# Kernel tuning notes

Measured on AMD Instinct MI355X. Metric: run time of the kernel, lower is better.

Reference implementation:

```python
import jax, jax.numpy as jnp
import numpy as np

B, S, H = 2, 2048, 2048
NH, NKV, HD = 16, 4, 128  # heads, kv heads, head_dim
GROUP = NH // NKV
THETA = 10000.0
NEG = -1e9


def _rope_tables(seq_len, head_dim, theta):
    inv_freq = 1.0 / (theta ** (jnp.arange(0, head_dim, 2, dtype=jnp.float32) / head_dim))
    t = jnp.arange(seq_len, dtype=jnp.float32)
    freqs = jnp.outer(t, inv_freq)                 # [S, HD/2]
    emb = jnp.concatenate([freqs, freqs], axis=-1)  # [S, HD]
    return jnp.cos(emb), jnp.sin(emb)


def _rotate_half(x):
    half = x.shape[-1] // 2
    return jnp.concatenate([-x[..., half:], x[..., :half]], axis=-1)


def setup_inputs() -> dict:
    key = jax.random.key(0)
    ks = jax.random.split(key, 5)
    scale = 0.02
    x = jax.random.normal(ks[0], (B, S, H), dtype=jnp.float32)
    Wq = jax.random.normal(ks[1], (NH * HD, H), dtype=jnp.float32) * scale
    Wk = jax.random.normal(ks[2], (NKV * HD, H), dtype=jnp.float32) * scale
    Wv = jax.random.normal(ks[3], (NKV * HD, H), dtype=jnp.float32) * scale
    Wo = jax.random.normal(ks[4], (H, NH * HD), dtype=jnp.float32) * scale
    cos, sin = _rope_tables(S, HD, THETA)
    # additive causal mask: 0 on/below diagonal, -1e9 above
    causal = jnp.triu(jnp.full((S, S), NEG, dtype=jnp.float32), k=1)
    mask = causal[None, None]  # [1,1,S,S]
    return {"x": x, "Wq": Wq, "Wk": Wk, "Wv": Wv, "Wo": Wo,
            "cos": cos, "sin": sin, "mask": mask}


def reference(x, Wq, Wk, Wv, Wo, cos, sin, mask):
    b, s, _ = x.shape
    # projections (nn.Linear, no bias): y = x @ W.T
    q = (x @ Wq.T).reshape(b, s, NH, HD).transpose(0, 2, 1, 3)    # [B,NH,S,D]
    k = (x @ Wk.T).reshape(b, s, NKV, HD).transpose(0, 2, 1, 3)   # [B,NKV,S,D]
    v = (x @ Wv.T).reshape(b, s, NKV, HD).transpose(0, 2, 1, 3)   # [B,NKV,S,D]
    # RoPE
    c = cos[None, None]  # [1,1,S,D]
    sn = sin[None, None]
    q = q * c + _rotate_half(q) * sn
    k = k * c + _rotate_half(k) * sn
    # GQA: repeat KV heads to match query heads (mirrors _repeat_kv)
    k = jnp.repeat(k, GROUP, axis=1)  # [B,NH,S,D]
    v = jnp.repeat(v, GROUP, axis=1)
    # scaled dot-product attention with additive mask
    scores = jnp.einsum('bhqd,bhkd->bhqk', q, k) / jnp.sqrt(jnp.float32(HD))
    scores = scores + mask
    p = jax.nn.softmax(scores, axis=-1)
    ctx = jnp.einsum('bhqk,bhkd->bhqd', p, v)            # [B,NH,S,D]
    ctx = ctx.transpose(0, 2, 1, 3).reshape(b, s, NH * HD)
    return ctx @ Wo.T
```

## Files before the change

### kernel.cpp

```cpp
#include <hip/hip_runtime.h>
#include <stdint.h>

#define B_   2
#define S_   2048
#define H_   2048
#define NH_  16
#define NKV_ 4
#define HD_  128
#define M_   (B_ * S_)

typedef short bf16x8 __attribute__((ext_vector_type(8)));
typedef float f32x4  __attribute__((ext_vector_type(4)));
typedef float f32x16 __attribute__((ext_vector_type(16)));

__device__ __forceinline__ float b2f(unsigned short u) {
  union { unsigned int u; float f; } v; v.u = ((unsigned int)u) << 16; return v.f;
}
__device__ __forceinline__ unsigned short f2b(float f) {
  union { float f; unsigned int u; } v; v.f = f;
  unsigned int u = v.u;
  unsigned int r = (u + 0x7FFFu + ((u >> 16) & 1u)) >> 16;
  return (unsigned short)r;
}
__device__ __forceinline__ uint4 pack8(const float4& a, const float4& b) {
  uint4 r;
  r.x = (unsigned)f2b(a.x) | ((unsigned)f2b(a.y) << 16);
  r.y = (unsigned)f2b(a.z) | ((unsigned)f2b(a.w) << 16);
  r.z = (unsigned)f2b(b.x) | ((unsigned)f2b(b.y) << 16);
  r.w = (unsigned)f2b(b.z) | ((unsigned)f2b(b.w) << 16);
  return r;
}
__device__ __forceinline__ void gload_lds(const unsigned short* g, unsigned short* l) {
  __builtin_amdgcn_global_load_lds(
      (const __attribute__((address_space(1))) unsigned int*)g,
      (__attribute__((address_space(3))) unsigned int*)l, 16, 0, 0);
}

__global__ void cvt_bf16(const float* __restrict__ src, unsigned short* __restrict__ dst, int n8)
{
  int i = blockIdx.x * blockDim.x + threadIdx.x;
  if (i >= n8) return;
  const float* p = src + (size_t)i * 8;
  uint4 v = pack8(*reinterpret_cast<const float4*>(p), *reinterpret_cast<const float4*>(p + 4));
  *reinterpret_cast<uint4*>(dst + (size_t)i * 8) = v;
}

template<bool CF32>
__global__ __launch_bounds__(256, 4) void gemm_ld(
    const unsigned short* __restrict__ A, const unsigned short* __restrict__ B0,
    const unsigned short* __restrict__ B1, void* __restrict__ C0, void* __restrict__ C1,
    int N, int K, int nxHalf)
{
  __shared__ unsigned short As[128 * 64];
  __shared__ unsigned short Bs[128 * 64];

  const unsigned short* Bm; void* Cm; int colBase;
  if ((int)blockIdx.x < nxHalf) { Bm = B0; Cm = C0; colBase = blockIdx.x * 128; }
  else                          { Bm = B1; Cm = C1; colBase = (blockIdx.x - nxHalf) * 128; }
  const int rowBase = blockIdx.y * 128;

  const int tid    = threadIdx.x;
  const int lane   = tid & 63;
  const int wid    = tid >> 6;
  const int wrow   = wid >> 1;
  const int wcol   = wid & 1;
  const int lane15 = lane & 15;
  const int quad   = lane >> 4;

  const f32x4 zero = {0.f, 0.f, 0.f, 0.f};
  f32x4 acc[4][4];
#pragma unroll
  for (int i = 0; i < 4; i++)
#pragma unroll
    for (int j = 0; j < 4; j++) acc[i][j] = zero;

  const int lr  = lane >> 3;
  const int sc8 = (lane & 7) ^ lr;

  for (int kb = 0; kb < K; kb += 64) {
    __syncthreads();
#pragma unroll
    for (int i = 0; i < 4; i++) {
      const int rg = (i * 4 + wid) * 8;
      const int r  = rg + lr;
      gload_lds(A  + (size_t)(rowBase + r) * K + kb + sc8 * 8, As + rg * 64);
      gload_lds(Bm + (size_t)(colBase + r) * K + kb + sc8 * 8, Bs + rg * 64);
    }
    __syncthreads();
#pragma unroll
    for (int kc = 0; kc < 2; kc++) {
      bf16x8 af[4], bf[4];
#pragma unroll
      for (int g = 0; g < 4; g++) {
        const int ra = wrow * 64 + g * 16 + lane15;
        const int rb = wcol * 64 + g * 16 + lane15;
        af[g] = *reinterpret_cast<const bf16x8*>(As + ra * 64 + (((kc * 4 + quad) ^ (ra & 7)) * 8));
        bf[g] = *reinterpret_cast<const bf16x8*>(Bs + rb * 64 + (((kc * 4 + quad) ^ (rb & 7)) * 8));
      }
#pragma unroll
      for (int i = 0; i < 4; i++)
#pragma unroll
        for (int j = 0; j < 4; j++)
          acc[i][j] = __builtin_amdgcn_mfma_f32_16x16x32_bf16(af[i], bf[j], acc[i][j], 0, 0, 0);
    }
  }

  if (CF32) {
    float* Cf = (float*)Cm;
#pragma unroll
    for (int i = 0; i < 4; i++) {
      int row = rowBase + wrow * 64 + i * 16 + quad * 4;
#pragma unroll
      for (int j = 0; j < 4; j++) {
        int col = colBase + wcol * 64 + j * 16 + lane15;
#pragma unroll
        for (int rr = 0; rr < 4; rr++)
          Cf[(size_t)(row + rr) * N + col] = acc[i][j][rr];
      }
    }
  } else {
    unsigned short* Cb = (unsigned short*)Cm;
#pragma unroll
    for (int i = 0; i < 4; i++) {
      int row = rowBase + wrow * 64 + i * 16 + quad * 4;
#pragma unroll
      for (int j = 0; j < 4; j++) {
        int col = colBase + wcol * 64 + j * 16 + lane15;
#pragma unroll
        for (int rr = 0; rr < 4; rr++)
          Cb[(size_t)(row + rr) * N + col] = f2b(acc[i][j][rr]);
      }
    }
  }
}

template<bool OPROJ>
__global__ __launch_bounds__(256, 3) void gemm_k(
    const void* __restrict__ A, const float* __restrict__ B0, const float* __restrict__ B1,
    void* __restrict__ C0, void* __restrict__ C1, int N, int K, int nxHalf)
{
  __shared__ unsigned short As[128 * 72];
  __shared__ unsigned short Bs[128 * 72];

  const float* Bm; void* Cm; int colBase;
  if ((int)blockIdx.x < nxHalf) { Bm = B0; Cm = C0; colBase = blockIdx.x * 128; }
  else                          { Bm = B1; Cm = C1; colBase = (blockIdx.x - nxHalf) * 128; }
  const int rowBase = blockIdx.y * 128;

  const int tid    = threadIdx.x;
  const int lane   = tid & 63;
  const int wid    = tid >> 6;
  const int wrow   = wid >> 1;
  const int wcol   = wid & 1;
  const int lane15 = lane & 15;
  const int quad   = lane >> 4;

  const f32x4 zero = {0.f, 0.f, 0.f, 0.f};
  f32x4 acc[4][4];
#pragma unroll
  for (int i = 0; i < 4; i++)
#pragma unroll
    for (int j = 0; j < 4; j++) acc[i][j] = zero;

  const int r0 = tid >> 3;
  const int c8 = tid & 7;

  uint4 av[4], bv[4];
#pragma unroll
  for (int p = 0; p < 4; p++) {
    int r = r0 + 32 * p;
    if (OPROJ) {
      av[p] = *reinterpret_cast<const uint4*>((const unsigned short*)A + (size_t)(rowBase + r) * K + c8 * 8);
    } else {
      const float* pA = (const float*)A + (size_t)(rowBase + r) * K + c8 * 8;
      av[p] = pack8(*reinterpret_cast<const float4*>(pA), *reinterpret_cast<const float4*>(pA + 4));
    }
    const float* pB = Bm + (size_t)(colBase + r) * K + c8 * 8;
    bv[p] = pack8(*reinterpret_cast<const float4*>(pB), *reinterpret_cast<const float4*>(pB + 4));
  }

  for (int kb = 0; kb < K; kb += 64) {
    __syncthreads();
#pragma unroll
    for (int p = 0; p < 4; p++) {
      int r = r0 + 32 * p;
      *reinterpret_cast<uint4*>(As + r * 72 + c8 * 8) = av[p];
      *reinterpret_cast<uint4*>(Bs + r * 72 + c8 * 8) = bv[p];
    }
    __syncthreads();
    const int kn = kb + 64;
    if (kn < K) {
#pragma unroll
      for (int p = 0; p < 4; p++) {
        int r = r0 + 32 * p;
        if (OPROJ) {
          av[p] = *reinterpret_cast<const uint4*>((const unsigned short*)A + (size_t)(rowBase + r) * K + kn + c8 * 8);
        } else {
          const float* pA = (const float*)A + (size_t)(rowBase + r) * K + kn + c8 * 8;
          av[p] = pack8(*reinterpret_cast<const float4*>(pA), *reinterpret_cast<const float4*>(pA + 4));
        }
        const float* pB = Bm + (size_t)(colBase + r) * K + kn + c8 * 8;
        bv[p] = pack8(*reinterpret_cast<const float4*>(pB), *reinterpret_cast<const float4*>(pB + 4));
      }
    }
#pragma unroll
    for (int kc = 0; kc < 2; kc++) {
      bf16x8 af[4], bf[4];
#pragma unroll
      for (int g = 0; g < 4; g++) {
        af[g] = *reinterpret_cast<const bf16x8*>(As + (wrow * 64 + g * 16 + lane15) * 72 + kc * 32 + quad * 8);
        bf[g] = *reinterpret_cast<const bf16x8*>(Bs + (wcol * 64 + g * 16 + lane15) * 72 + kc * 32 + quad * 8);
      }
#pragma unroll
      for (int i = 0; i < 4; i++)
#pragma unroll
        for (int j = 0; j < 4; j++)
          acc[i][j] = __builtin_amdgcn_mfma_f32_16x16x32_bf16(af[i], bf[j], acc[i][j], 0, 0, 0);
    }
  }

  if (OPROJ) {
    float* Cf = (float*)Cm;
#pragma unroll
    for (int i = 0; i < 4; i++) {
      int row = rowBase + wrow * 64 + i * 16 + quad * 4;
#pragma unroll
      for (int j = 0; j < 4; j++) {
        int col = colBase + wcol * 64 + j * 16 + lane15;
#pragma unroll
        for (int rr = 0; rr < 4; rr++)
          Cf[(size_t)(row + rr) * N + col] = acc[i][j][rr];
      }
    }
  } else {
    unsigned short* Cb = (unsigned short*)Cm;
#pragma unroll
    for (int i = 0; i < 4; i++) {
      int row = rowBase + wrow * 64 + i * 16 + quad * 4;
#pragma unroll
      for (int j = 0; j < 4; j++) {
        int col = colBase + wcol * 64 + j * 16 + lane15;
#pragma unroll
        for (int rr = 0; rr < 4; rr++)
          Cb[(size_t)(row + rr) * N + col] = f2b(acc[i][j][rr]);
      }
    }
  }
}

__global__ void rope_k(unsigned short* __restrict__ Qb, unsigned short* __restrict__ Kb,
                       const float* __restrict__ cosT, const float* __restrict__ sinT)
{
  const int per_tok = (NH_ + NKV_) * 64;
  int idx = blockIdx.x * blockDim.x + threadIdx.x;
  int t = idx / per_tok;
  int r = idx - t * per_tok;
  if (t >= M_) return;
  int s = t & (S_ - 1);
  unsigned short* base;
  int d;
  if (r < NH_ * 64) {
    int h = r >> 6; d = r & 63;
    base = Qb + (size_t)t * (NH_ * HD_) + h * HD_ + d;
  } else {
    int rk = r - NH_ * 64;
    int h = rk >> 6; d = rk & 63;
    base = Kb + (size_t)t * (NKV_ * HD_) + h * HD_ + d;
  }
  float c  = cosT[s * HD_ + d];
  float sn = sinT[s * HD_ + d];
  float x0 = b2f(base[0]);
  float x1 = b2f(base[64]);
  base[0]  = f2b(x0 * c - x1 * sn);
  base[64] = f2b(x1 * c + x0 * sn);
}

__global__ void transp_v(const unsigned short* __restrict__ Vb, unsigned short* __restrict__ VT)
{
  __shared__ unsigned short Ls[64 * 72];
  const int t0 = blockIdx.x * 64;
  const int d0 = blockIdx.y * 64;
  const int tid = threadIdx.x;
  const int r = tid >> 3, c = tid & 7;
#pragma unroll
  for (int p = 0; p < 2; p++)
    *reinterpret_cast<uint4*>(Ls + (r + 32 * p) * 72 + c * 8) =
      *reinterpret_cast<const uint4*>(Vb + (size_t)(t0 + r + 32 * p) * (NKV_ * HD_) + d0 + c * 8);
  __syncthreads();
  const int bq = t0 >> 11, s0 = t0 & (S_ - 1);
#pragma unroll
  for (int p = 0; p < 2; p++) {
    int dl = r + 32 * p;
    unsigned short tmp[8];
#pragma unroll
    for (int j = 0; j < 8; j++) tmp[j] = Ls[(c * 8 + j) * 72 + dl];
    *reinterpret_cast<uint4*>(VT + (size_t)(bq * 512 + d0 + dl) * S_ + s0 + c * 8) =
      *reinterpret_cast<uint4*>(tmp);
  }
}

__global__ __launch_bounds__(512, 2) void attn(
    const unsigned short* __restrict__ Q, const unsigned short* __restrict__ Kc,
    const unsigned short* __restrict__ VT, unsigned short* __restrict__ O)
{
  __shared__ unsigned short Ks[64 * 128];
  __shared__ unsigned short Vs[128 * 64];
  __shared__ float Ll[8 * 32];

  const int tid  = threadIdx.x;
  const int lane = tid & 63;
  const int w    = tid >> 6;
  const int l31  = lane & 31;
  const int hi   = lane >> 5;
  const int qt   = blockIdx.x;
  const int kvh  = blockIdx.y;
  const int b    = blockIdx.z;
  const int h    = kvh * 4 + (w & 3);
  const int rg   = w >> 2;
  const size_t bS = (size_t)b * S_;
  const int ntot = qt + 1;

  const int kr   = tid >> 4;
  const int kc16 = tid & 15;
  const int vd   = tid >> 3;
  const int vc8  = tid & 7;

  const unsigned short* Kbase = Kc + bS * (NKV_ * HD_) + kvh * HD_;
  const unsigned short* Vbase = VT + (size_t)(b * 512 + kvh * HD_) * S_;

  bf16x8 qf[8];
  {
    const unsigned short* qp = Q + (bS + qt * 64 + rg * 32 + l31) * (NH_ * HD_) + h * HD_ + hi * 8;
#pragma unroll
    for (int kc = 0; kc < 8; kc++) qf[kc] = *reinterpret_cast<const bf16x8*>(qp + kc * 16);
  }

  f32x16 ctx[4];
#pragma unroll
  for (int ng = 0; ng < 4; ng++)
#pragma unroll
    for (int r = 0; r < 16; r++) ctx[ng][r] = 0.f;
  float lsum = 0.f;

  uint4 kreg[2], vreg[2];
#pragma unroll
  for (int p2 = 0; p2 < 2; p2++) {
    kreg[p2] = *reinterpret_cast<const uint4*>(Kbase + (size_t)(kr + 32 * p2) * (NKV_ * HD_) + kc16 * 8);
    vreg[p2] = *reinterpret_cast<const uint4*>(Vbase + (size_t)(vd + 64 * p2) * S_ + vc8 * 8);
  }

  const float scale = 0.08838834764831845f;

  for (int kt = 0; kt < ntot; kt++) {
    __syncthreads();
#pragma unroll
    for (int p2 = 0; p2 < 2; p2++) {
      const int row = kr + 32 * p2;
      *reinterpret_cast<uint4*>(Ks + row * 128 + ((kc16 ^ (row & 15)) * 8)) = kreg[p2];
      const int d = vd + 64 * p2;
      *reinterpret_cast<uint4*>(Vs + d * 64 + ((vc8 ^ (d & 7)) * 8)) = vreg[p2];
    }
    __syncthreads();

    if (kt + 1 < ntot) {
      const int key0 = (kt + 1) * 64;
#pragma unroll
      for (int p2 = 0; p2 < 2; p2++) {
        kreg[p2] = *reinterpret_cast<const uint4*>(Kbase + (size_t)(key0 + kr + 32 * p2) * (NKV_ * HD_) + kc16 * 8);
        vreg[p2] = *reinterpret_cast<const uint4*>(Vbase + (size_t)(vd + 64 * p2) * S_ + key0 + vc8 * 8);
      }
    }

    f32x16 sc0, sc1;
#pragma unroll
    for (int r = 0; r < 16; r++) { sc0[r] = 0.f; sc1[r] = 0.f; }
#pragma unroll
    for (int kc = 0; kc < 8; kc++) {
      const int ch = ((kc * 2 + hi) ^ (l31 & 15)) * 8;
      bf16x8 kf0 = *reinterpret_cast<const bf16x8*>(Ks + l31 * 128 + ch);
      sc0 = __builtin_amdgcn_mfma_f32_32x32x16_bf16(kf0, qf[kc], sc0, 0, 0, 0);
      bf16x8 kf1 = *reinterpret_cast<const bf16x8*>(Ks + (32 + l31) * 128 + ch);
      sc1 = __builtin_amdgcn_mfma_f32_32x32x16_bf16(kf1, qf[kc], sc1, 0, 0, 0);
    }

    const int lim = (kt == qt) ? (rg * 32 + l31) : 4096;
    bf16x8 pfrag[4];
#pragma unroll
    for (int cg = 0; cg < 2; cg++) {
      float pe[16];
#pragma unroll
      for (int r = 0; r < 16; r++) {
        float v = (cg ? sc1[r] : sc0[r]) * scale;
        const int kp = cg * 32 + (r & 3) + 8 * (r >> 2) + 4 * hi;
        v = (kp <= lim) ? v : -1.0e9f;
        float e = __expf(v);
        pe[r] = e;
        lsum += e;
      }
      unsigned wd[8];
#pragma unroll
      for (int j = 0; j < 8; j++) {
        unsigned t;
        asm("v_cvt_pk_bf16_f32 %0, %1, %2" : "=v"(t) : "v"(pe[2 * j]), "v"(pe[2 * j + 1]));
        wd[j] = t;
      }
      asm("v_permlane32_swap_b32 %0, %1" : "+v"(wd[0]), "+v"(wd[2]));
      asm("v_permlane32_swap_b32 %0, %1" : "+v"(wd[1]), "+v"(wd[3]));
      asm("v_permlane32_swap_b32 %0, %1" : "+v"(wd[4]), "+v"(wd[6]));
      asm("v_permlane32_swap_b32 %0, %1" : "+v"(wd[5]), "+v"(wd[7]));
      union { unsigned u[4]; bf16x8 v8; } ua, ub;
      ua.u[0] = wd[0]; ua.u[1] = wd[1]; ua.u[2] = wd[2]; ua.u[3] = wd[3];
      ub.u[0] = wd[4]; ub.u[1] = wd[5]; ub.u[2] = wd[6]; ub.u[3] = wd[7];
      pfrag[cg * 2]     = ua.v8;
      pfrag[cg * 2 + 1] = ub.v8;
    }

#pragma unroll
    for (int ng = 0; ng < 4; ng++) {
      const int drow = ng * 32 + l31;
#pragma unroll
      for (int kc = 0; kc < 4; kc++) {
        bf16x8 vf = *reinterpret_cast<const bf16x8*>(Vs + drow * 64 + (((kc * 2 + hi) ^ (l31 & 7)) * 8));
        ctx[ng] = __builtin_amdgcn_mfma_f32_32x32x16_bf16(pfrag[kc], vf, ctx[ng], 0, 0, 0);
      }
    }
  }

  {
    float lt = lsum + __shfl_xor(lsum, 32);
    Ll[w * 32 + l31] = 1.0f / lt;
  }
  f32x4 iv[4];
#pragma unroll
  for (int g = 0; g < 4; g++)
    iv[g] = *reinterpret_cast<const f32x4*>(&Ll[w * 32 + 4 * hi + 8 * g]);

  const size_t orow0 = bS + qt * 64 + rg * 32;
#pragma unroll
  for (int ng = 0; ng < 4; ng++) {
#pragma unroll
    for (int r = 0; r < 16; r++) {
      const int qp = (r & 3) + 8 * (r >> 2) + 4 * hi;
      O[(orow0 + qp) * (NH_ * HD_) + h * HD_ + ng * 32 + l31] = f2b(ctx[ng][r] * iv[r >> 2][r & 3]);
    }
  }
}

extern "C" void kernel_launch(void* const* d_in, const int* in_sizes, int n_in,
                              void* d_out, int out_size, void* d_ws, size_t ws_size,
                              hipStream_t stream) {
  const float* x    = (const float*)d_in[0];
  const float* Wq   = (const float*)d_in[1];
  const float* Wk   = (const float*)d_in[2];
  const float* Wv   = (const float*)d_in[3];
  const float* Wo   = (const float*)d_in[4];
  const float* cosT = (const float*)d_in[5];
  const float* sinT = (const float*)d_in[6];
  float* out = (float*)d_out;

  const size_t qElems  = (size_t)M_ * NH_ * HD_;
  const size_t xElems  = (size_t)M_ * H_;
  const size_t wqElems = (size_t)H_ * H_;
  const size_t wkElems = (size_t)NKV_ * HD_ * H_;
  const size_t bigNeed = (qElems + xElems + 2 * wqElems + 2 * wkElems) * 2 + 256;

  if (ws_size < qElems * 2 + 256) return;

  unsigned short* Qb = (unsigned short*)d_ws;
  unsigned short* Kb = (unsigned short*)d_out;
  unsigned short* Vb = Kb + (size_t)M_ * NKV_ * HD_;
  unsigned short* VT = Vb + (size_t)M_ * NKV_ * HD_;

  dim3 blk(256);
  const int rope_threads = M_ * (NH_ + NKV_) * 64;

  if (ws_size >= bigNeed) {
    unsigned short* xb  = Qb + qElems;
    unsigned short* Wqb = xb + xElems;
    unsigned short* Wob = Wqb + wqElems;
    unsigned short* Wkb = Wob + wqElems;
    unsigned short* Wvb = Wkb + wkElems;

    cvt_bf16<<<dim3((int)(xElems / 8 + 255) / 256), blk, 0, stream>>>(x,  xb,  (int)(xElems / 8));
    cvt_bf16<<<dim3((int)(wqElems / 8 + 255) / 256), blk, 0, stream>>>(Wq, Wqb, (int)(wqElems / 8));
    cvt_bf16<<<dim3((int)(wkElems / 8 + 255) / 256), blk, 0, stream>>>(Wk, Wkb, (int)(wkElems / 8));
    cvt_bf16<<<dim3((int)(wkElems / 8 + 255) / 256), blk, 0, stream>>>(Wv, Wvb, (int)(wkElems / 8));
    cvt_bf16<<<dim3((int)(wqElems / 8 + 255) / 256), blk, 0, stream>>>(Wo, Wob, (int)(wqElems / 8));

    gemm_ld<false><<<dim3(16, 32), blk, 0, stream>>>(xb, Wqb, Wqb, Qb, Qb, NH_ * HD_, H_, 16);
    gemm_ld<false><<<dim3(8, 32), blk, 0, stream>>>(xb, Wkb, Wvb, Kb, Vb, NKV_ * HD_, H_, 4);

    rope_k<<<dim3((rope_threads + 255) / 256), blk, 0, stream>>>(Qb, Kb, cosT, sinT);
    transp_v<<<dim3(M_ / 64, (NKV_ * HD_) / 64), blk, 0, stream>>>(Vb, VT);
    attn<<<dim3(32, NKV_, B_), dim3(512), 0, stream>>>(Qb, Kb, VT, Qb);

    gemm_ld<true><<<dim3(16, 32), blk, 0, stream>>>(Qb, Wob, Wob, out, out, H_, NH_ * HD_, 16);
  } else {
    gemm_k<false><<<dim3(16, 32), blk, 0, stream>>>(x, Wq, Wq, Qb, Qb, NH_ * HD_, H_, 16);
    gemm_k<false><<<dim3(8, 32), blk, 0, stream>>>(x, Wk, Wv, Kb, Vb, NKV_ * HD_, H_, 4);

    rope_k<<<dim3((rope_threads + 255) / 256), blk, 0, stream>>>(Qb, Kb, cosT, sinT);
    transp_v<<<dim3(M_ / 64, (NKV_ * HD_) / 64), blk, 0, stream>>>(Vb, VT);
    attn<<<dim3(32, NKV_, B_), dim3(512), 0, stream>>>(Qb, Kb, VT, Qb);

    gemm_k<true><<<dim3(16, 32), blk, 0, stream>>>(Qb, Wo, Wo, out, out, H_, NH_ * HD_, 16);
  }
}
```

Before: 394.0 us.

## Double-buffer K/V tiles in LDS and raise MFMA wave priority in attention

The attention kernel now uses two LDS buffers for the K and V tiles, so the next tile is written while the current one is consumed. This needs only one barrier per iteration instead of two. MFMA sections are wrapped in s_setprio to favour matrix issue, and the final normalization uses lane shuffles instead of an LDS scratch array. LDS use doubles, and launch bounds drop to one block per CU (512 threads), which may reduce occupancy.

```diff
diff --git a/kernel.cpp b/kernel.cpp
--- a/kernel.cpp
+++ b/kernel.cpp
@@ -299,26 +299,26 @@
   }
 }
 
-__global__ __launch_bounds__(512, 2) void attn(
+__global__ __launch_bounds__(512, 1) void attn(
     const unsigned short* __restrict__ Q, const unsigned short* __restrict__ Kc,
     const unsigned short* __restrict__ VT, unsigned short* __restrict__ O)
 {
-  __shared__ unsigned short Ks[64 * 128];
-  __shared__ unsigned short Vs[128 * 64];
-  __shared__ float Ll[8 * 32];
+  __shared__ unsigned short KsA[2 * 64 * 128];
+  __shared__ unsigned short VsA[2 * 128 * 64];
 
   const int tid  = threadIdx.x;
   const int lane = tid & 63;
   const int w    = tid >> 6;
   const int l31  = lane & 31;
   const int hi   = lane >> 5;
-  const int qt   = blockIdx.x;
+  const int g    = blockIdx.x;
   const int kvh  = blockIdx.y;
   const int b    = blockIdx.z;
   const int h    = kvh * 4 + (w & 3);
   const int rg   = w >> 2;
   const size_t bS = (size_t)b * S_;
-  const int ntot = qt + 1;
+  const int nkt  = g + 1;
+  const int qb   = g * 64;
 
   const int kr   = tid >> 4;
   const int kc16 = tid & 15;
@@ -330,7 +330,7 @@
 
   bf16x8 qf[8];
   {
-    const unsigned short* qp = Q + (bS + qt * 64 + rg * 32 + l31) * (NH_ * HD_) + h * HD_ + hi * 8;
+    const unsigned short* qp = Q + (bS + qb + rg * 32 + l31) * (NH_ * HD_) + h * HD_ + hi * 8;
 #pragma unroll
     for (int kc = 0; kc < 8; kc++) qf[kc] = *reinterpret_cast<const bf16x8*>(qp + kc * 16);
   }
@@ -341,6 +341,8 @@
 #pragma unroll
     for (int r = 0; r < 16; r++) ctx[ng][r] = 0.f;
   float lsum = 0.f;
+
+  const float scale = 0.08838834764831845f;
 
   uint4 kreg[2], vreg[2];
 #pragma unroll
@@ -348,21 +350,22 @@
     kreg[p2] = *reinterpret_cast<const uint4*>(Kbase + (size_t)(kr + 32 * p2) * (NKV_ * HD_) + kc16 * 8);
     vreg[p2] = *reinterpret_cast<const uint4*>(Vbase + (size_t)(vd + 64 * p2) * S_ + vc8 * 8);
   }
-
-  const float scale = 0.08838834764831845f;
-
-  for (int kt = 0; kt < ntot; kt++) {
-    __syncthreads();
-#pragma unroll
-    for (int p2 = 0; p2 < 2; p2++) {
-      const int row = kr + 32 * p2;
-      *reinterpret_cast<uint4*>(Ks + row * 128 + ((kc16 ^ (row & 15)) * 8)) = kreg[p2];
-      const int d = vd + 64 * p2;
-      *reinterpret_cast<uint4*>(Vs + d * 64 + ((vc8 ^ (d & 7)) * 8)) = vreg[p2];
-    }
-    __syncthreads();
-
-    if (kt + 1 < ntot) {
+#pragma unroll
+  for (int p2 = 0; p2 < 2; p2++) {
+    const int row = kr + 32 * p2;
+    *reinterpret_cast<uint4*>(KsA + row * 128 + ((kc16 ^ (row & 15)) * 8)) = kreg[p2];
+    const int d = vd + 64 * p2;
+    *reinterpret_cast<uint4*>(VsA + d * 64 + ((vc8 ^ (d & 7)) * 8)) = vreg[p2];
+  }
+  __syncthreads();
+
+  for (int kt = 0; kt < nkt; kt++) {
+    unsigned short* ksc = KsA + (kt & 1) * 8192;
+    unsigned short* vsc = VsA + (kt & 1) * 8192;
+    unsigned short* ksn = KsA + ((kt & 1) ^ 1) * 8192;
+    unsigned short* vsn = VsA + ((kt & 1) ^ 1) * 8192;
+
+    if (kt + 1 < nkt) {
       const int key0 = (kt + 1) * 64;
 #pragma unroll
       for (int p2 = 0; p2 < 2; p2++) {
@@ -374,16 +377,18 @@
     f32x16 sc0, sc1;
 #pragma unroll
     for (int r = 0; r < 16; r++) { sc0[r] = 0.f; sc1[r] = 0.f; }
+    __builtin_amdgcn_s_setprio(1);
 #pragma unroll
     for (int kc = 0; kc < 8; kc++) {
       const int ch = ((kc * 2 + hi) ^ (l31 & 15)) * 8;
-      bf16x8 kf0 = *reinterpret_cast<const bf16x8*>(Ks + l31 * 128 + ch);
+      bf16x8 kf0 = *reinterpret_cast<const bf16x8*>(ksc + l31 * 128 + ch);
       sc0 = __builtin_amdgcn_mfma_f32_32x32x16_bf16(kf0, qf[kc], sc0, 0, 0, 0);
-      bf16x8 kf1 = *reinterpret_cast<const bf16x8*>(Ks + (32 + l31) * 128 + ch);
+      bf16x8 kf1 = *reinterpret_cast<const bf16x8*>(ksc + (32 + l31) * 128 + ch);
       sc1 = __builtin_amdgcn_mfma_f32_32x32x16_bf16(kf1, qf[kc], sc1, 0, 0, 0);
     }
-
-    const int lim = (kt == qt) ? (rg * 32 + l31) : 4096;
+    __builtin_amdgcn_s_setprio(0);
+
+    const int lim = (kt == nkt - 1) ? (rg * 32 + l31) : 4096;
     bf16x8 pfrag[4];
 #pragma unroll
     for (int cg = 0; cg < 2; cg++) {
@@ -415,34 +420,45 @@
       pfrag[cg * 2 + 1] = ub.v8;
     }
 
+    __builtin_amdgcn_s_setprio(1);
 #pragma unroll
     for (int ng = 0; ng < 4; ng++) {
       const int drow = ng * 32 + l31;
 #pragma unroll
       for (int kc = 0; kc < 4; kc++) {
-        bf16x8 vf = *reinterpret_cast<const bf16x8*>(Vs + drow * 64 + (((kc * 2 + hi) ^ (l31 & 7)) * 8));
+        bf16x8 vf = *reinterpret_cast<const bf16x8*>(vsc + drow * 64 + (((kc * 2 + hi) ^ (l31 & 7)) * 8));
         ctx[ng] = __builtin_amdgcn_mfma_f32_32x32x16_bf16(pfrag[kc], vf, ctx[ng], 0, 0, 0);
       }
     }
+    __builtin_amdgcn_s_setprio(0);
+
+    if (kt + 1 < nkt) {
+#pragma unroll
+      for (int p2 = 0; p2 < 2; p2++) {
+        const int row = kr + 32 * p2;
+        *reinterpret_cast<uint4*>(ksn + row * 128 + ((kc16 ^ (row & 15)) * 8)) = kreg[p2];
+        const int d = vd + 64 * p2;
+        *reinterpret_cast<uint4*>(vsn + d * 64 + ((vc8 ^ (d & 7)) * 8)) = vreg[p2];
+      }
+      __syncthreads();
+    }
   }
 
   {
-    float lt = lsum + __shfl_xor(lsum, 32);
-    Ll[w * 32 + l31] = 1.0f / lt;
-  }
-  f32x4 iv[4];
-#pragma unroll
-  for (int g = 0; g < 4; g++)
-    iv[g] = *reinterpret_cast<const f32x4*>(&Ll[w * 32 + 4 * hi + 8 * g]);
-
-  const size_t orow0 = bS + qt * 64 + rg * 32;
-#pragma unroll
-  for (int ng = 0; ng < 4; ng++) {
-#pragma unroll
-    for (int r = 0; r < 16; r++) {
-      const int qp = (r & 3) + 8 * (r >> 2) + 4 * hi;
-      O[(orow0 + qp) * (NH_ * HD_) + h * HD_ + ng * 32 + l31] = f2b(ctx[ng][r] * iv[r >> 2][r & 3]);
-    }
+    float lt  = lsum + __shfl_xor(lsum, 32);
+    float inv = 1.0f / lt;
+    float il[16];
+#pragma unroll
+    for (int r = 0; r < 16; r++)
+      il[r] = __shfl(inv, (r & 3) + 8 * (r >> 2) + 4 * hi);
+    const size_t orow0 = bS + qb + rg * 32;
+#pragma unroll
+    for (int ng = 0; ng < 4; ng++)
+#pragma unroll
+      for (int r = 0; r < 16; r++) {
+        const int qp = (r & 3) + 8 * (r >> 2) + 4 * hi;
+        O[(orow0 + qp) * (NH_ * HD_) + h * HD_ + ng * 32 + l31] = f2b(ctx[ng][r] * il[r]);
+      }
   }
 }
 
```

Result: faster. 364.7 us (-7.4%).
